# Kernel tuning notes

Hardware: AMD Instinct MI355X
Metric: run time of the kernel (lower is better)

Reference implementation:

```python
import jax, jax.numpy as jnp
import numpy as np

N, E = 100000, 1600000
IN_F, HID, OUT_F, HEADS = 256, 128, 64, 1
C = HID // HEADS  # per-head channels (=128 for heads=1)
NEG_SLOPE = 0.2   # PyG GATConv default leaky_relu slope


def setup_inputs() -> dict:
    key = jax.random.key(0)
    ks = jax.random.split(key, 16)
    w = lambda k, shape, fan: (jax.random.normal(k, shape, jnp.float32) / np.float32(np.sqrt(fan)))
    return {
        "x": jax.random.normal(ks[0], (N, IN_F), jnp.float32),
        "edge_index": jax.random.randint(ks[1], (2, E), 0, N, dtype=jnp.int32),
        "W_in": w(ks[2], (IN_F, HID), IN_F),
        "b_in": jnp.zeros((HID,), jnp.float32),
        "W1": w(ks[3], (HID, HEADS * C), HID),
        "att_src1": w(ks[4], (HEADS, C), C),
        "att_dst1": w(ks[5], (HEADS, C), C),
        "bias1": jnp.zeros((C,), jnp.float32),
        "W2": w(ks[6], (HID, HEADS * C), HID),
        "att_src2": w(ks[7], (HEADS, C), C),
        "att_dst2": w(ks[8], (HEADS, C), C),
        "bias2": jnp.zeros((C,), jnp.float32),
        "W_out": w(ks[9], (HID, OUT_F), HID),
        "b_out": jnp.zeros((OUT_F,), jnp.float32),
    }


def gat_conv(h, src, dst, W, a_src, a_dst, bias):
    """PyG GATConv, concat=False: per-head attention, segment softmax over dst, mean over heads."""
    g = (h @ W).reshape(-1, HEADS, C)                      # [N,H,C]
    alpha_src = jnp.einsum("nhc,hc->nh", g, a_src)         # [N,H]
    alpha_dst = jnp.einsum("nhc,hc->nh", g, a_dst)         # [N,H]
    e = jax.nn.leaky_relu(alpha_src[src] + alpha_dst[dst], NEG_SLOPE)  # [E,H]
    m = jax.ops.segment_max(e, dst, num_segments=N)        # [N,H], -inf for empty segments
    m = jnp.where(jnp.isfinite(m), m, 0.0)
    p = jnp.exp(e - m[dst])
    s = jax.ops.segment_sum(p, dst, num_segments=N)        # [N,H]
    alpha = p / (s[dst] + 1e-16)                           # [E,H]
    msg = g[src] * alpha[..., None]                        # [E,H,C]  (dominant traffic)
    out = jax.ops.segment_sum(msg, dst, num_segments=N)    # [N,H,C]
    return out.mean(axis=1) + bias                         # concat=False -> head average


def reference(x, edge_index, W_in, b_in, W1, att_src1, att_dst1, bias1,
              W2, att_src2, att_dst2, bias2, W_out, b_out):
    src, dst = edge_index[0], edge_index[1]
    h = x @ W_in + b_in
    h = jax.nn.relu(gat_conv(h, src, dst, W1, att_src1, att_dst1, bias1))
    h = jax.nn.relu(gat_conv(h, src, dst, W2, att_src2, att_dst2, bias2))
    return h @ W_out + b_out
```

## Files before the change

### kernel.cpp

```cpp
#include <hip/hip_runtime.h>
#include <hip/hip_fp16.h>
#include <math.h>

#define NN 100000
#define EE 1600000
constexpr int IN_F = 256, HID = 128, OUT_F = 64;

#define NB 196
#define CAP 16384
#define CH 4096
#define NCHUNK 391

typedef __bf16    bf16x8 __attribute__((ext_vector_type(8)));
typedef _Float16  h16x8  __attribute__((ext_vector_type(8)));
typedef float     f32x4  __attribute__((ext_vector_type(4)));

__device__ __forceinline__ f32x4 mfma16b(bf16x8 a, bf16x8 b, f32x4 c){
  return __builtin_amdgcn_mfma_f32_16x16x32_bf16(a, b, c, 0, 0, 0);
}
__device__ __forceinline__ f32x4 mfma16h(h16x8 a, h16x8 b, f32x4 c){
  return __builtin_amdgcn_mfma_f32_16x16x32_f16(a, b, c, 0, 0, 0);
}

__device__ __forceinline__ void fmamix2(float& aLo, float& aHi, __half2 g2, float al){
  asm("v_fma_mix_f32 %0, %2, %3, %0 op_sel:[0,0,0] op_sel_hi:[1,0,0]\n\t"
      "v_fma_mix_f32 %1, %2, %3, %1 op_sel:[1,0,0] op_sel_hi:[1,0,0]"
      : "+v"(aLo), "+v"(aHi) : "v"(g2), "v"(al));
}

__device__ __forceinline__ float wred_max(float v){
#pragma unroll
  for (int m=1; m<64; m<<=1) v = fmaxf(v, __shfl_xor(v, m, 64));
  return v;
}
__device__ __forceinline__ float wred_sum(float v){
#pragma unroll
  for (int m=1; m<64; m<<=1) v += __shfl_xor(v, m, 64);
  return v;
}

__device__ __forceinline__ unsigned fkey(float x){
  unsigned u = __float_as_uint(x);
  return (u & 0x80000000u) ? ~u : (u ^ 0x80000000u);
}
__device__ __forceinline__ float funkey(unsigned k){
  return __uint_as_float((k & 0x80000000u) ? (k ^ 0x80000000u) : ~k);
}

__global__ __launch_bounds__(256) void k_bin(const int* __restrict__ src,
    const int* __restrict__ dst, int* __restrict__ bucketCnt, int* __restrict__ recs)
{
  __shared__ int cnt[NB];
  __shared__ int base[NB];
  const int tid = threadIdx.x;
  const int e0 = blockIdx.x * CH;
  const int ne = min(CH, EE - e0);

  for (int i=tid; i<NB; i+=256) cnt[i] = 0;
  __syncthreads();
  for (int i=tid; i<ne; i+=256) atomicAdd(&cnt[dst[e0+i]>>9], 1);
  __syncthreads();
  for (int i=tid; i<NB; i+=256) base[i] = atomicAdd(&bucketCnt[i], cnt[i]);
  __syncthreads();
  for (int i=tid; i<NB; i+=256) cnt[i] = 0;
  __syncthreads();
  for (int i=tid; i<ne; i+=256){
    int d = dst[e0+i], b = d >> 9;
    int r = atomicAdd(&cnt[b], 1);
    int pos = base[b] + r;
    if (pos < CAP) recs[(size_t)b*CAP + pos] = src[e0+i] | ((d & 511) << 17);
  }
}

__global__ void k_bscan(const int* __restrict__ bucketCnt, int* __restrict__ bucketStart){
  __shared__ int sd[256];
  int t = threadIdx.x;
  int v = (t < NB) ? min(bucketCnt[t], CAP) : 0;
  sd[t] = v; __syncthreads();
#pragma unroll
  for (int off=1; off<256; off<<=1){
    int x = (t >= off) ? sd[t-off] : 0;
    __syncthreads();
    sd[t] += x;
    __syncthreads();
  }
  if (t < NB) bucketStart[t] = sd[t] - v;
}

__global__ __launch_bounds__(512) void k_csr(const int* __restrict__ recs,
    const int* __restrict__ bucketCnt, const int* __restrict__ bucketStart,
    int* __restrict__ rp, int* __restrict__ colsrc)
{
  __shared__ int hist[513];
  __shared__ int srcbuf[CAP];
  const int tid = threadIdx.x;
  const int b = blockIdx.x;
  const int cntb = min(bucketCnt[b], CAP);
  const int bstart = bucketStart[b];
  const int n0 = b << 9;
  const int nnode = min(512, NN - n0);
  const int* rb = recs + (size_t)b*CAP;

  if (tid < 513) hist[tid] = 0;
  if (tid == 511) hist[512] = 0;
  __syncthreads();
  for (int i=tid; i<cntb; i+=512) atomicAdd(&hist[(rb[i] >> 17) + 1], 1);
  __syncthreads();
#pragma unroll
  for (int off=1; off<513; off<<=1){
    int v0 = (tid >= off) ? hist[tid-off] : 0;
    int i1 = tid + 512;
    int v1 = (i1 < 513 && i1 >= off) ? hist[i1-off] : 0;
    __syncthreads();
    hist[tid] += v0;
    if (i1 < 513) hist[i1] += v1;
    __syncthreads();
  }
  for (int l=tid; l<nnode; l+=512) rp[n0+l] = bstart + hist[l];
  if (b == 0 && tid == 0) rp[NN] = EE;
  __syncthreads();
  for (int i=tid; i<cntb; i+=512){
    int rec = rb[i];
    int r = atomicAdd(&hist[rec >> 17], 1);
    srcbuf[r] = rec & 0x1FFFF;
  }
  __syncthreads();
  for (int i=tid; i<cntb; i+=512) colsrc[bstart + i] = srcbuf[i];
}

__global__ void k_wsplit_all(
    const float* __restrict__ W_in, __bf16* __restrict__ whiI, __bf16* __restrict__ wloI,
    const float* __restrict__ W1, _Float16* __restrict__ w1h, _Float16* __restrict__ w1l,
    const float* __restrict__ W2, _Float16* __restrict__ w2h, _Float16* __restrict__ w2l,
    const float* __restrict__ W_out, _Float16* __restrict__ wOh, _Float16* __restrict__ wOl)
{
  int idx = blockIdx.x*256 + threadIdx.x;
  if (idx < 32768){
    int k = idx >> 7, n = idx & 127;
    float v = W_in[idx];
    __bf16 h = (__bf16)v;
    whiI[n*256 + k] = h;
    wloI[n*256 + k] = (__bf16)(v - (float)h);
  } else if (idx < 49152){
    int i = idx - 32768, k = i >> 7, n = i & 127;
    float v = W1[i] * 16.f;
    _Float16 h = (_Float16)v;
    w1h[n*128 + k] = h;
    w1l[n*128 + k] = (_Float16)(v - (float)h);
  } else if (idx < 65536){
    int i = idx - 49152, k = i >> 7, n = i & 127;
    float v = W2[i] * 16.f;
    _Float16 h = (_Float16)v;
    w2h[n*128 + k] = h;
    w2l[n*128 + k] = (_Float16)(v - (float)h);
  } else if (idx < 73728){
    int i = idx - 65536, k = i / 64, n = i - k*64;
    float v = W_out[i] * 16.f;
    _Float16 h = (_Float16)v;
    wOh[n*128 + k] = h;
    wOl[n*128 + k] = (_Float16)(v - (float)h);
  }
}

__global__ __launch_bounds__(256, 2) void k_gemm_in(
    const float* __restrict__ A, const __bf16* __restrict__ Bhi, const __bf16* __restrict__ Blo,
    const float* __restrict__ bias, __half* __restrict__ C, int nrows)
{
  constexpr int K = 256, BN = 128, NF = 8;
  __shared__ __bf16 Ah[256][36];
  __shared__ __bf16 Al[256][36];
  __shared__ __bf16 Bh[BN][36];
  __shared__ __bf16 Bl[BN][36];
  const int tid = threadIdx.x, w = tid >> 6, lane = tid & 63;
  const int lr = lane & 15, lk = (lane >> 4) * 8;
  const int rowBase = blockIdx.x * 256;

  f32x4 acc[4][NF];
#pragma unroll
  for (int f=0; f<4; f++)
#pragma unroll
    for (int nf=0; nf<NF; nf++) acc[f][nf] = (f32x4)(0.f);

  const int bn = tid >> 1, bo = (tid & 1) * 16;

  for (int kc=0; kc<K; kc+=32){
    float4 av[8];
#pragma unroll
    for (int k8=0; k8<8; k8++){
      int P = tid + 256*k8;
      int r = P >> 3, pc = P & 7;
      int gr = rowBase + r; if (gr >= nrows) gr = nrows - 1;
      av[k8] = *(const float4*)(A + (size_t)gr*K + kc + pc*4);
    }
    bf16x8 bh0, bh1, bl0, bl1;
    {
      const __bf16* ph = Bhi + (size_t)bn*K + kc + bo;
      const __bf16* pl = Blo + (size_t)bn*K + kc + bo;
      bh0 = *(const bf16x8*)(ph);  bh1 = *(const bf16x8*)(ph + 8);
      bl0 = *(const bf16x8*)(pl);  bl1 = *(const bf16x8*)(pl + 8);
    }
    __syncthreads();
#pragma unroll
    for (int k8=0; k8<8; k8++){
      int P = tid + 256*k8;
      int r = P >> 3, pc = P & 7;
      float fv[4] = {av[k8].x, av[k8].y, av[k8].z, av[k8].w};
      __bf16 h4[4], l4[4];
#pragma unroll
      for (int u=0; u<4; u++){
        __bf16 h = (__bf16)fv[u];
        h4[u] = h; l4[u] = (__bf16)(fv[u] - (float)h);
      }
      *(uint2*)&Ah[r][pc*4] = *(uint2*)h4;
      *(uint2*)&Al[r][pc*4] = *(uint2*)l4;
    }
    *(bf16x8*)&Bh[bn][bo]     = bh0;  *(bf16x8*)&Bh[bn][bo + 8] = bh1;
    *(bf16x8*)&Bl[bn][bo]     = bl0;  *(bf16x8*)&Bl[bn][bo + 8] = bl1;
    __syncthreads();

    bf16x8 fah[4], fal[4];
#pragma unroll
    for (int f=0; f<4; f++){
      fah[f] = *(const bf16x8*)&Ah[w*64 + f*16 + lr][lk];
      fal[f] = *(const bf16x8*)&Al[w*64 + f*16 + lr][lk];
    }
#pragma unroll
    for (int nf=0; nf<NF; nf++){
      bf16x8 bh = *(const bf16x8*)&Bh[nf*16 + lr][lk];
#pragma unroll
      for (int f=0; f<4; f++) acc[f][nf] = mfma16b(fah[f], bh, acc[f][nf]);
#pragma unroll
      for (int f=0; f<4; f++) acc[f][nf] = mfma16b(fal[f], bh, acc[f][nf]);
      bf16x8 bl = *(const bf16x8*)&Bl[nf*16 + lr][lk];
#pragma unroll
      for (int f=0; f<4; f++) acc[f][nf] = mfma16b(fah[f], bl, acc[f][nf]);
    }
  }

  const int rq = lane >> 4;
#pragma unroll
  for (int f=0; f<4; f++){
    const int rbase = rowBase + w*64 + f*16 + rq*4;
#pragma unroll
    for (int i=0; i<4; i++){
      int row = rbase + i;
      if (row < nrows){
#pragma unroll
        for (int nf=0; nf<NF; nf++){
          float v = acc[f][nf][i] + bias[nf*16 + lr];
          C[(size_t)row*BN + nf*16 + lr] = __float2half(v);
        }
      }
    }
  }
}

template<int K, int BN, bool ATT, bool BIAS, int OMODE>
__global__ __launch_bounds__(256, 2) void k_gemm_f16(
    const _Float16* __restrict__ A, const _Float16* __restrict__ Whi,
    const _Float16* __restrict__ Wlo, const float* __restrict__ bias,
    void* __restrict__ C0, const float* __restrict__ attS, const float* __restrict__ attD,
    float* __restrict__ asrc, float* __restrict__ adst,
    unsigned* __restrict__ gk, int nrows)
{
  constexpr int NF = BN/16;
  __shared__ _Float16 Ah[256][40];
  __shared__ _Float16 Bh[BN][40];
  __shared__ _Float16 Bl[BN][40];
  const int tid = threadIdx.x, w = tid >> 6, lane = tid & 63;
  const int lr = lane & 15, lk = (lane >> 4) * 8;
  const int rowBase = blockIdx.x * 256;

  f32x4 acc[4][NF];
#pragma unroll
  for (int f=0; f<4; f++)
#pragma unroll
    for (int nf=0; nf<NF; nf++) acc[f][nf] = (f32x4)(0.f);

  const bool bact = tid < BN*2;
  const int bn = tid >> 1, bo = (tid & 1) * 16;

  for (int kc=0; kc<K; kc+=32){
    h16x8 av[4];
#pragma unroll
    for (int k4=0; k4<4; k4++){
      int P = tid + 256*k4;
      int r = P >> 2, pc = P & 3;
      int gr = rowBase + r; if (gr >= nrows) gr = nrows - 1;
      av[k4] = *(const h16x8*)(A + (size_t)gr*K + kc + pc*8);
    }
    h16x8 bh0, bh1, bl0, bl1;
    if (bact){
      const _Float16* ph = Whi + (size_t)bn*K + kc + bo;
      const _Float16* pl = Wlo + (size_t)bn*K + kc + bo;
      bh0 = *(const h16x8*)(ph);  bh1 = *(const h16x8*)(ph + 8);
      bl0 = *(const h16x8*)(pl);  bl1 = *(const h16x8*)(pl + 8);
    }
    __syncthreads();
#pragma unroll
    for (int k4=0; k4<4; k4++){
      int P = tid + 256*k4;
      int r = P >> 2, pc = P & 3;
      *(h16x8*)&Ah[r][pc*8] = av[k4];
    }
    if (bact){
      *(h16x8*)&Bh[bn][bo]     = bh0;  *(h16x8*)&Bh[bn][bo + 8] = bh1;
      *(h16x8*)&Bl[bn][bo]     = bl0;  *(h16x8*)&Bl[bn][bo + 8] = bl1;
    }
    __syncthreads();

    h16x8 fah[4];
#pragma unroll
    for (int f=0; f<4; f++) fah[f] = *(const h16x8*)&Ah[w*64 + f*16 + lr][lk];
#pragma unroll
    for (int nf=0; nf<NF; nf++){
      h16x8 bh = *(const h16x8*)&Bh[nf*16 + lr][lk];
#pragma unroll
      for (int f=0; f<4; f++) acc[f][nf] = mfma16h(fah[f], bh, acc[f][nf]);
      h16x8 bl = *(const h16x8*)&Bl[nf*16 + lr][lk];
#pragma unroll
      for (int f=0; f<4; f++) acc[f][nf] = mfma16h(fah[f], bl, acc[f][nf]);
    }
  }
#pragma unroll
  for (int f=0; f<4; f++)
#pragma unroll
    for (int nf=0; nf<NF; nf++) acc[f][nf] *= 0.0625f;

  const int rq = lane >> 4;
  float pmax = -3e38f;
#pragma unroll
  for (int f=0; f<4; f++){
    const int rbase = rowBase + w*64 + f*16 + rq*4;
    if (ATT){
      float ps[4] = {0.f,0.f,0.f,0.f}, pd[4] = {0.f,0.f,0.f,0.f};
#pragma unroll
      for (int nf=0; nf<NF; nf++){
        float sv = attS[nf*16 + lr], dv = attD[nf*16 + lr];
#pragma unroll
        for (int i=0;i<4;i++){
          ps[i] = fmaf(acc[f][nf][i], sv, ps[i]);
          pd[i] = fmaf(acc[f][nf][i], dv, pd[i]);
        }
      }
#pragma unroll
      for (int mm=1; mm<16; mm<<=1){
#pragma unroll
        for (int i=0;i<4;i++){
          ps[i] += __shfl_xor(ps[i], mm, 64);
          pd[i] += __shfl_xor(pd[i], mm, 64);
        }
      }
      if (lr == 0){
#pragma unroll
        for (int i=0;i<4;i++){
          int row = rbase + i;
          if (row < nrows){ asrc[row] = ps[i]; adst[row] = pd[i]; }
        }
        pmax = fmaxf(pmax, fmaxf(fmaxf(ps[0],ps[1]), fmaxf(ps[2],ps[3])));
      }
    }
#pragma unroll
    for (int i=0;i<4;i++){
      int row = rbase + i;
      if (row < nrows){
#pragma unroll
        for (int nf=0; nf<NF; nf++){
          float v = acc[f][nf][i] + (BIAS ? bias[nf*16 + lr] : 0.f);
          size_t cidx = (size_t)row*BN + nf*16 + lr;
          if constexpr (OMODE == 0) ((float*)C0)[cidx] = v;
          else                      ((__half*)C0)[cidx] = __float2half(v);
        }
      }
    }
  }
  if (ATT){
    pmax = wred_max(pmax);
    if (lane == 0) atomicMax(gk, fkey(pmax));
  }
}

__global__ __launch_bounds__(512) void k_alpha(
    const float* __restrict__ asrc, const float* __restrict__ adst,
    const int* __restrict__ rp, const int* __restrict__ cs,
    const unsigned* __restrict__ gkey, int2* __restrict__ epack)
{
  int w = threadIdx.x >> 6, lane = threadIdx.x & 63;
  int node = blockIdx.x*8 + w;
  if (node >= NN) return;
  int r0 = rp[node], deg = rp[node+1] - r0;
  if (deg == 0) return;
  float ad = adst[node];
  float tC = funkey(*gkey) + ad;
  float C = (tC > 0.f) ? tC : 0.2f*tC;

  float p0 = 0.f, p1 = 0.f; int s0 = 0, s1 = 0;
  float ssum = 0.f;
  for (int i = lane; i < deg; i += 64){
    int s = cs[r0 + i];
    float t = asrc[s] + ad;
    float e = (t > 0.f) ? t : 0.2f*t;
    float p = __expf(e - C);
    ssum += p;
    if (i < 64)       { p0 = p; s0 = s; }
    else if (i < 128) { p1 = p; s1 = s; }
  }
  ssum = wred_sum(ssum);
  float inv = 1.f/(ssum + 1e-16f);
  if (lane < deg)      epack[r0 + lane]      = make_int2(s0, __float_as_int(p0*inv));
  if (64 + lane < deg) epack[r0 + 64 + lane] = make_int2(s1, __float_as_int(p1*inv));
  for (int i = 128 + lane; i < deg; i += 64){
    int s = cs[r0 + i];
    float t = asrc[s] + ad;
    float e = (t > 0.f) ? t : 0.2f*t;
    epack[r0 + i] = make_int2(s, __float_as_int(__expf(e - C)*inv));
  }
}

__global__ __launch_bounds__(512) void k_gather(const __half* __restrict__ g,
    const int2* __restrict__ epack, const int* __restrict__ rp,
    const float* __restrict__ bias, __half* __restrict__ out)
{
  int w = threadIdx.x >> 6, lane = threadIdx.x & 63;
  int node = blockIdx.x*8 + w;
  if (node >= NN) return;
  int r0 = rp[node], deg = rp[node+1] - r0;
  const int eg = lane >> 4, cl = lane & 15;
  const __half* gcl = g + cl*8;
  const int2* ep = epack + r0 + eg;

  float a[8] = {0.f,0.f,0.f,0.f,0.f,0.f,0.f,0.f};
  int nst = (deg + 3) >> 2;

  int2 e0 = make_int2(0,0), e1 = e0, e2 = e0, e3 = e0;
  if (0 < nst && eg < deg)        e0 = ep[0];
  if (1 < nst && 4  + eg < deg)   e1 = ep[4];
  if (2 < nst && 8  + eg < deg)   e2 = ep[8];
  if (3 < nst && 12 + eg < deg)   e3 = ep[12];
  float4 g0 = *(const float4*)(gcl + ((size_t)((unsigned)e0.x << 7)));
  float4 g1 = *(const float4*)(gcl + ((size_t)((unsigned)e1.x << 7)));
  float4 g2 = *(const float4*)(gcl + ((size_t)((unsigned)e2.x << 7)));
  float4 g3 = *(const float4*)(gcl + ((size_t)((unsigned)e3.x << 7)));

#define GSTEP(EV, GV, SOFF)                                                  \
  {                                                                          \
    float al = __int_as_float(EV.y); float4 cur = GV;                        \
    int nj = j + 4 + SOFF;                                                   \
    if (nj < nst){                                                           \
      int idx = 4*nj + eg;                                                   \
      EV = (idx < deg) ? ep[4*nj] : make_int2(0,0);                          \
      GV = *(const float4*)(gcl + ((size_t)((unsigned)EV.x << 7)));          \
    }                                                                        \
    const __half2* hp = (const __half2*)&cur;                                \
    fmamix2(a[0], a[1], hp[0], al);                                          \
    fmamix2(a[2], a[3], hp[1], al);                                          \
    fmamix2(a[4], a[5], hp[2], al);                                          \
    fmamix2(a[6], a[7], hp[3], al);                                          \
  }

  for (int j = 0; j < nst; j += 4){
    GSTEP(e0, g0, 0)
    if (j + 1 < nst) GSTEP(e1, g1, 1)
    if (j + 2 < nst) GSTEP(e2, g2, 2)
    if (j + 3 < nst) GSTEP(e3, g3, 3)
  }
#undef GSTEP

#pragma unroll
  for (int u=0; u<8; u++){
    a[u] += __shfl_xor(a[u], 16, 64);
    a[u] += __shfl_xor(a[u], 32, 64);
  }
  if (eg == 0){
    __half hv[8];
#pragma unroll
    for (int u=0; u<8; u++)
      hv[u] = __float2half(fmaxf(a[u] + bias[cl*8 + u], 0.f));
    *(float4*)(out + (size_t)node*HID + cl*8) = *(float4*)hv;
  }
}

extern "C" void kernel_launch(void* const* d_in, const int* in_sizes, int n_in,
                              void* d_out, int out_size, void* d_ws, size_t ws_size,
                              hipStream_t stream) {
  const float* x     = (const float*)d_in[0];
  const int*   ei    = (const int*)  d_in[1];
  const float* W_in  = (const float*)d_in[2];
  const float* b_in  = (const float*)d_in[3];
  const float* W1    = (const float*)d_in[4];
  const float* as1   = (const float*)d_in[5];
  const float* ad1   = (const float*)d_in[6];
  const float* bias1 = (const float*)d_in[7];
  const float* W2    = (const float*)d_in[8];
  const float* as2   = (const float*)d_in[9];
  const float* ad2   = (const float*)d_in[10];
  const float* bias2 = (const float*)d_in[11];
  const float* W_out = (const float*)d_in[12];
  const float* b_out = (const float*)d_in[13];
  float* out = (float*)d_out;

  char* ws = (char*)d_ws;
  size_t off = 0;
  auto alloc = [&](size_t bytes)->void*{ void* p = ws + off; off += (bytes + 255) & ~255ull; return p; };
  __half*   H    = (__half*)  alloc((size_t)NN*HID*2);
  __half*   G    = (__half*)  alloc((size_t)NN*HID*2);
  __half*   O1   = (__half*)  alloc((size_t)NN*HID*2);
  float*    asrc = (float*)   alloc((size_t)NN*4);
  float*    adst = (float*)   alloc((size_t)NN*4);
  int*      rp   = (int*)     alloc((size_t)(NN+1)*4);
  int*      colsrc = (int*)   alloc((size_t)EE*4);
  int2*     epack  = (int2*)  alloc((size_t)EE*8);
  int*      recs   = (int*)   alloc((size_t)NB*CAP*4);
  int*      misc   = (int*)   alloc((size_t)(NB+2)*4);
  int*      bucketCnt = misc;
  unsigned* gk1 = (unsigned*)(misc + NB);
  unsigned* gk2 = (unsigned*)(misc + NB + 1);
  int*      bucketStart = (int*)alloc(NB*4);
  __bf16*   whiI = (__bf16*) alloc((size_t)HID*IN_F*2);
  __bf16*   wloI = (__bf16*) alloc((size_t)HID*IN_F*2);
  _Float16* w1h  = (_Float16*)alloc((size_t)HID*HID*2);
  _Float16* w1l  = (_Float16*)alloc((size_t)HID*HID*2);
  _Float16* w2h  = (_Float16*)alloc((size_t)HID*HID*2);
  _Float16* w2l  = (_Float16*)alloc((size_t)HID*HID*2);
  _Float16* wOh  = (_Float16*)alloc((size_t)OUT_F*HID*2);
  _Float16* wOl  = (_Float16*)alloc((size_t)OUT_F*HID*2);
  (void)ws_size; (void)in_sizes; (void)n_in; (void)out_size;

  const int* srcIdx = ei;
  const int* dstIdx = ei + EE;

  k_wsplit_all<<<288, 256, 0, stream>>>(W_in, whiI, wloI, W1, w1h, w1l, W2, w2h, w2l, W_out, wOh, wOl);
  hipMemsetAsync(misc, 0, (size_t)(NB+2)*4, stream);

  k_bin  <<<NCHUNK, 256, 0, stream>>>(srcIdx, dstIdx, bucketCnt, recs);
  k_bscan<<<1, 256, 0, stream>>>(bucketCnt, bucketStart);
  k_csr  <<<NB, 512, 0, stream>>>(recs, bucketCnt, bucketStart, rp, colsrc);

  const int gblocks = (NN + 255) / 256;
  const int ablocks = (NN + 7) / 8;
  k_gemm_in<<<gblocks, 256, 0, stream>>>(x, whiI, wloI, b_in, H, NN);
  k_gemm_f16<128,128,true,false,1><<<gblocks, 256, 0, stream>>>(
      (const _Float16*)H, w1h, w1l, nullptr, G, as1, ad1, asrc, adst, gk1, NN);
  k_alpha <<<ablocks, 512, 0, stream>>>(asrc, adst, rp, colsrc, gk1, epack);
  k_gather<<<ablocks, 512, 0, stream>>>(G, epack, rp, bias1, O1);
  k_gemm_f16<128,128,true,false,1><<<gblocks, 256, 0, stream>>>(
      (const _Float16*)O1, w2h, w2l, nullptr, G, as2, ad2, asrc, adst, gk2, NN);
  k_alpha <<<ablocks, 512, 0, stream>>>(asrc, adst, rp, colsrc, gk2, epack);
  k_gather<<<ablocks, 512, 0, stream>>>(G, epack, rp, bias2, (__half*)H);
  k_gemm_f16<128,64,false,true,0><<<gblocks, 256, 0, stream>>>(
      (const _Float16*)H, wOh, wOl, b_out, out, nullptr, nullptr, nullptr, nullptr, nullptr, NN);
}
```

Before: 339.1 us.

## Fuse attention softmax into gather and fold bucket scan into CSR build

Merges the alpha and gather kernels into one per-node kernel. It computes unnormalized attention weights into a per-wave LDS buffer in 128-edge chunks, gathers features, and normalizes once at the end by the summed weights. This removes the 1.6M-entry epack write and re-read and two launches per layer. It also drops the separate bucket-scan kernel by having each CSR block serially sum preceding bucket counts, and keeps dst values in registers in k_bin to avoid reloading them. In exchange, the LDS staging and serial prefix add some latency per wave and per block.

```diff
diff --git a/kernel.cpp b/kernel.cpp
--- a/kernel.cpp
+++ b/kernel.cpp
@@ -58,52 +58,55 @@
 
   for (int i=tid; i<NB; i+=256) cnt[i] = 0;
   __syncthreads();
-  for (int i=tid; i<ne; i+=256) atomicAdd(&cnt[dst[e0+i]>>9], 1);
+  int d[16];
+#pragma unroll
+  for (int q=0; q<16; q++){
+    int i = tid + q*256;
+    d[q] = (i < ne) ? dst[e0+i] : -1;
+    if (d[q] >= 0) atomicAdd(&cnt[d[q]>>9], 1);
+  }
   __syncthreads();
   for (int i=tid; i<NB; i+=256) base[i] = atomicAdd(&bucketCnt[i], cnt[i]);
   __syncthreads();
   for (int i=tid; i<NB; i+=256) cnt[i] = 0;
   __syncthreads();
-  for (int i=tid; i<ne; i+=256){
-    int d = dst[e0+i], b = d >> 9;
-    int r = atomicAdd(&cnt[b], 1);
-    int pos = base[b] + r;
-    if (pos < CAP) recs[(size_t)b*CAP + pos] = src[e0+i] | ((d & 511) << 17);
-  }
-}
-
-__global__ void k_bscan(const int* __restrict__ bucketCnt, int* __restrict__ bucketStart){
-  __shared__ int sd[256];
-  int t = threadIdx.x;
-  int v = (t < NB) ? min(bucketCnt[t], CAP) : 0;
-  sd[t] = v; __syncthreads();
-#pragma unroll
-  for (int off=1; off<256; off<<=1){
-    int x = (t >= off) ? sd[t-off] : 0;
-    __syncthreads();
-    sd[t] += x;
-    __syncthreads();
-  }
-  if (t < NB) bucketStart[t] = sd[t] - v;
+#pragma unroll
+  for (int q=0; q<16; q++){
+    int i = tid + q*256;
+    if (d[q] >= 0){
+      int b = d[q] >> 9;
+      int r = atomicAdd(&cnt[b], 1);
+      int pos = base[b] + r;
+      if (pos < CAP) recs[(size_t)b*CAP + pos] = src[e0+i] | ((d[q] & 511) << 17);
+    }
+  }
 }
 
 __global__ __launch_bounds__(512) void k_csr(const int* __restrict__ recs,
-    const int* __restrict__ bucketCnt, const int* __restrict__ bucketStart,
-    int* __restrict__ rp, int* __restrict__ colsrc)
+    const int* __restrict__ bucketCnt, int* __restrict__ rp, int* __restrict__ colsrc)
 {
+  __shared__ int scnt[NB];
   __shared__ int hist[513];
   __shared__ int srcbuf[CAP];
+  __shared__ int bs_sh;
   const int tid = threadIdx.x;
   const int b = blockIdx.x;
-  const int cntb = min(bucketCnt[b], CAP);
-  const int bstart = bucketStart[b];
+  for (int i=tid; i<NB; i+=512) scnt[i] = min(bucketCnt[i], CAP);
+  if (tid < 513) hist[tid] = 0;
+  if (tid == 0) hist[512] = 0;
+  __syncthreads();
+  if (tid == 0){
+    int acc = 0;
+    for (int i=0; i<b; i++) acc += scnt[i];
+    bs_sh = acc;
+  }
+  __syncthreads();
+  const int bstart = bs_sh;
+  const int cntb = scnt[b];
   const int n0 = b << 9;
   const int nnode = min(512, NN - n0);
   const int* rb = recs + (size_t)b*CAP;
 
-  if (tid < 513) hist[tid] = 0;
-  if (tid == 511) hist[512] = 0;
-  __syncthreads();
   for (int i=tid; i<cntb; i+=512) atomicAdd(&hist[(rb[i] >> 17) + 1], 1);
   __syncthreads();
 #pragma unroll
@@ -380,102 +383,87 @@
   }
 }
 
-__global__ __launch_bounds__(512) void k_alpha(
+__global__ __launch_bounds__(512) void k_agg2(const __half* __restrict__ g,
     const float* __restrict__ asrc, const float* __restrict__ adst,
     const int* __restrict__ rp, const int* __restrict__ cs,
-    const unsigned* __restrict__ gkey, int2* __restrict__ epack)
+    const float* __restrict__ bias, const unsigned* __restrict__ gkey,
+    __half* __restrict__ out)
 {
+  __shared__ int2 ebuf[8][128];
   int w = threadIdx.x >> 6, lane = threadIdx.x & 63;
   int node = blockIdx.x*8 + w;
   if (node >= NN) return;
   int r0 = rp[node], deg = rp[node+1] - r0;
-  if (deg == 0) return;
   float ad = adst[node];
   float tC = funkey(*gkey) + ad;
   float C = (tC > 0.f) ? tC : 0.2f*tC;
-
-  float p0 = 0.f, p1 = 0.f; int s0 = 0, s1 = 0;
-  float ssum = 0.f;
-  for (int i = lane; i < deg; i += 64){
-    int s = cs[r0 + i];
-    float t = asrc[s] + ad;
-    float e = (t > 0.f) ? t : 0.2f*t;
-    float p = __expf(e - C);
-    ssum += p;
-    if (i < 64)       { p0 = p; s0 = s; }
-    else if (i < 128) { p1 = p; s1 = s; }
-  }
-  ssum = wred_sum(ssum);
-  float inv = 1.f/(ssum + 1e-16f);
-  if (lane < deg)      epack[r0 + lane]      = make_int2(s0, __float_as_int(p0*inv));
-  if (64 + lane < deg) epack[r0 + 64 + lane] = make_int2(s1, __float_as_int(p1*inv));
-  for (int i = 128 + lane; i < deg; i += 64){
-    int s = cs[r0 + i];
-    float t = asrc[s] + ad;
-    float e = (t > 0.f) ? t : 0.2f*t;
-    epack[r0 + i] = make_int2(s, __float_as_int(__expf(e - C)*inv));
-  }
-}
-
-__global__ __launch_bounds__(512) void k_gather(const __half* __restrict__ g,
-    const int2* __restrict__ epack, const int* __restrict__ rp,
-    const float* __restrict__ bias, __half* __restrict__ out)
-{
-  int w = threadIdx.x >> 6, lane = threadIdx.x & 63;
-  int node = blockIdx.x*8 + w;
-  if (node >= NN) return;
-  int r0 = rp[node], deg = rp[node+1] - r0;
   const int eg = lane >> 4, cl = lane & 15;
   const __half* gcl = g + cl*8;
-  const int2* ep = epack + r0 + eg;
-
+  const int2* eb = &ebuf[w][eg];
+
+  float ssum = 0.f;
   float a[8] = {0.f,0.f,0.f,0.f,0.f,0.f,0.f,0.f};
-  int nst = (deg + 3) >> 2;
-
-  int2 e0 = make_int2(0,0), e1 = e0, e2 = e0, e3 = e0;
-  if (0 < nst && eg < deg)        e0 = ep[0];
-  if (1 < nst && 4  + eg < deg)   e1 = ep[4];
-  if (2 < nst && 8  + eg < deg)   e2 = ep[8];
-  if (3 < nst && 12 + eg < deg)   e3 = ep[12];
-  float4 g0 = *(const float4*)(gcl + ((size_t)((unsigned)e0.x << 7)));
-  float4 g1 = *(const float4*)(gcl + ((size_t)((unsigned)e1.x << 7)));
-  float4 g2 = *(const float4*)(gcl + ((size_t)((unsigned)e2.x << 7)));
-  float4 g3 = *(const float4*)(gcl + ((size_t)((unsigned)e3.x << 7)));
-
-#define GSTEP(EV, GV, SOFF)                                                  \
-  {                                                                          \
-    float al = __int_as_float(EV.y); float4 cur = GV;                        \
-    int nj = j + 4 + SOFF;                                                   \
-    if (nj < nst){                                                           \
-      int idx = 4*nj + eg;                                                   \
-      EV = (idx < deg) ? ep[4*nj] : make_int2(0,0);                          \
-      GV = *(const float4*)(gcl + ((size_t)((unsigned)EV.x << 7)));          \
-    }                                                                        \
-    const __half2* hp = (const __half2*)&cur;                                \
-    fmamix2(a[0], a[1], hp[0], al);                                          \
-    fmamix2(a[2], a[3], hp[1], al);                                          \
-    fmamix2(a[4], a[5], hp[2], al);                                          \
-    fmamix2(a[6], a[7], hp[3], al);                                          \
-  }
-
-  for (int j = 0; j < nst; j += 4){
-    GSTEP(e0, g0, 0)
-    if (j + 1 < nst) GSTEP(e1, g1, 1)
-    if (j + 2 < nst) GSTEP(e2, g2, 2)
-    if (j + 3 < nst) GSTEP(e3, g3, 3)
-  }
-#undef GSTEP
-
+
+  for (int base = 0; base < deg; base += 128){
+    int cnt = min(deg - base, 128);
+    int cpad = (cnt + 3) & ~3;
+    for (int i = lane; i < cpad; i += 64){
+      int s = 0; float p = 0.f;
+      if (i < cnt){
+        s = cs[r0 + base + i];
+        float t = asrc[s] + ad;
+        float e = (t > 0.f) ? t : 0.2f*t;
+        p = __expf(e - C);
+        ssum += p;
+      }
+      ebuf[w][i] = make_int2(s, __float_as_int(p));
+    }
+    int nst = cpad >> 2;
+    int2 e0 = eb[0];
+    int2 e1 = (1 < nst) ? eb[4]  : make_int2(0,0);
+    int2 e2 = (2 < nst) ? eb[8]  : make_int2(0,0);
+    int2 e3 = (3 < nst) ? eb[12] : make_int2(0,0);
+    float4 g0 = *(const float4*)(gcl + ((size_t)((unsigned)e0.x << 7)));
+    float4 g1 = *(const float4*)(gcl + ((size_t)((unsigned)e1.x << 7)));
+    float4 g2 = *(const float4*)(gcl + ((size_t)((unsigned)e2.x << 7)));
+    float4 g3 = *(const float4*)(gcl + ((size_t)((unsigned)e3.x << 7)));
+
+#define GSTEP2(EV, GV, SOFF)                                                 \
+    {                                                                        \
+      float al = __int_as_float(EV.y); float4 cur = GV;                      \
+      int nj = j + 4 + SOFF;                                                 \
+      if (nj < nst){                                                         \
+        EV = eb[4*nj];                                                       \
+        GV = *(const float4*)(gcl + ((size_t)((unsigned)EV.x << 7)));        \
+      }                                                                      \
+      const __half2* hp = (const __half2*)&cur;                              \
+      fmamix2(a[0], a[1], hp[0], al);                                        \
+      fmamix2(a[2], a[3], hp[1], al);                                        \
+      fmamix2(a[4], a[5], hp[2], al);                                        \
+      fmamix2(a[6], a[7], hp[3], al);                                        \
+    }
+
+    for (int j = 0; j < nst; j += 4){
+      GSTEP2(e0, g0, 0)
+      if (j + 1 < nst) GSTEP2(e1, g1, 1)
+      if (j + 2 < nst) GSTEP2(e2, g2, 2)
+      if (j + 3 < nst) GSTEP2(e3, g3, 3)
+    }
+#undef GSTEP2
+  }
+
+  ssum = wred_sum(ssum);
 #pragma unroll
   for (int u=0; u<8; u++){
     a[u] += __shfl_xor(a[u], 16, 64);
     a[u] += __shfl_xor(a[u], 32, 64);
   }
   if (eg == 0){
+    float inv = 1.f/(ssum + 1e-16f);
     __half hv[8];
 #pragma unroll
     for (int u=0; u<8; u++)
-      hv[u] = __float2half(fmaxf(a[u] + bias[cl*8 + u], 0.f));
+      hv[u] = __float2half(fmaxf(a[u]*inv + bias[cl*8 + u], 0.f));
     *(float4*)(out + (size_t)node*HID + cl*8) = *(float4*)hv;
   }
 }
@@ -509,13 +497,11 @@
   float*    adst = (float*)   alloc((size_t)NN*4);
   int*      rp   = (int*)     alloc((size_t)(NN+1)*4);
   int*      colsrc = (int*)   alloc((size_t)EE*4);
-  int2*     epack  = (int2*)  alloc((size_t)EE*8);
   int*      recs   = (int*)   alloc((size_t)NB*CAP*4);
   int*      misc   = (int*)   alloc((size_t)(NB+2)*4);
   int*      bucketCnt = misc;
   unsigned* gk1 = (unsigned*)(misc + NB);
   unsigned* gk2 = (unsigned*)(misc + NB + 1);
-  int*      bucketStart = (int*)alloc(NB*4);
   __bf16*   whiI = (__bf16*) alloc((size_t)HID*IN_F*2);
   __bf16*   wloI = (__bf16*) alloc((size_t)HID*IN_F*2);
   _Float16* w1h  = (_Float16*)alloc((size_t)HID*HID*2);
@@ -532,21 +518,18 @@
   k_wsplit_all<<<288, 256, 0, stream>>>(W_in, whiI, wloI, W1, w1h, w1l, W2, w2h, w2l, W_out, wOh, wOl);
   hipMemsetAsync(misc, 0, (size_t)(NB+2)*4, stream);
 
-  k_bin  <<<NCHUNK, 256, 0, stream>>>(srcIdx, dstIdx, bucketCnt, recs);
-  k_bscan<<<1, 256, 0, stream>>>(bucketCnt, bucketStart);
-  k_csr  <<<NB, 512, 0, stream>>>(recs, bucketCnt, bucketStart, rp, colsrc);
+  k_bin<<<NCHUNK, 256, 0, stream>>>(srcIdx, dstIdx, bucketCnt, recs);
+  k_csr<<<NB, 512, 0, stream>>>(recs, bucketCnt, rp, colsrc);
 
   const int gblocks = (NN + 255) / 256;
   const int ablocks = (NN + 7) / 8;
   k_gemm_in<<<gblocks, 256, 0, stream>>>(x, whiI, wloI, b_in, H, NN);
   k_gemm_f16<128,128,true,false,1><<<gblocks, 256, 0, stream>>>(
       (const _Float16*)H, w1h, w1l, nullptr, G, as1, ad1, asrc, adst, gk1, NN);
-  k_alpha <<<ablocks, 512, 0, stream>>>(asrc, adst, rp, colsrc, gk1, epack);
-  k_gather<<<ablocks, 512, 0, stream>>>(G, epack, rp, bias1, O1);
+  k_agg2<<<ablocks, 512, 0, stream>>>(G, asrc, adst, rp, colsrc, bias1, gk1, O1);
   k_gemm_f16<128,128,true,false,1><<<gblocks, 256, 0, stream>>>(
       (const _Float16*)O1, w2h, w2l, nullptr, G, as2, ad2, asrc, adst, gk2, NN);
-  k_alpha <<<ablocks, 512, 0, stream>>>(asrc, adst, rp, colsrc, gk2, epack);
-  k_gather<<<ablocks, 512, 0, stream>>>(G, epack, rp, bias2, (__half*)H);
+  k_agg2<<<ablocks, 512, 0, stream>>>(G, asrc, adst, rp, colsrc, bias2, gk2, (__half*)H);
   k_gemm_f16<128,64,false,true,0><<<gblocks, 256, 0, stream>>>(
       (const _Float16*)H, wOh, wOl, b_out, out, nullptr, nullptr, nullptr, nullptr, nullptr, NN);
 }
```

Result: faster. 290.7 us (-14.3%).
